# Optimization experiments

Hardware: AMD Instinct MI355X
Metric: run time of the kernel (lower is better)

## Reference

```python
import jax, jax.numpy as jnp
import numpy as np

N = 20000   # nodes
E = 160000  # edges
IN = 16     # in_channels
H = 32      # hidden_channels
MID = 32    # edge-MLP hidden width


def setup_inputs() -> dict:
    key = jax.random.key(0)
    ks = jax.random.split(key, 18)
    s = 0.1  # param scale
    return {
        "x": jax.random.normal(ks[0], (N, IN), jnp.float32),
        "edge_index": jax.random.randint(ks[1], (2, E), 0, N, dtype=jnp.int64),
        "edge_weight": jax.random.uniform(ks[2], (E,), jnp.float32),
        # edge_net1: Linear(1,32) -> SiLU -> Linear(32, IN*H)
        "en1_w1": jax.random.normal(ks[3], (1, MID), jnp.float32) * s,
        "en1_b1": jax.random.normal(ks[4], (MID,), jnp.float32) * s,
        "en1_w2": jax.random.normal(ks[5], (MID, IN * H), jnp.float32) * s,
        "en1_b2": jax.random.normal(ks[6], (IN * H,), jnp.float32) * s,
        "root1": jax.random.normal(ks[7], (IN, H), jnp.float32) * s,
        "bias1": jax.random.normal(ks[8], (H,), jnp.float32) * s,
        # edge_net2: Linear(1,32) -> SiLU -> Linear(32, H*H)
        "en2_w1": jax.random.normal(ks[9], (1, MID), jnp.float32) * s,
        "en2_b1": jax.random.normal(ks[10], (MID,), jnp.float32) * s,
        "en2_w2": jax.random.normal(ks[11], (MID, H * H), jnp.float32) * s,
        "en2_b2": jax.random.normal(ks[12], (H * H,), jnp.float32) * s,
        "root2": jax.random.normal(ks[13], (H, H), jnp.float32) * s,
        "bias2": jax.random.normal(ks[14], (H,), jnp.float32) * s,
        "dec_w": jax.random.normal(ks[15], (H, 1), jnp.float32) * s,
        "dec_b": jax.random.normal(ks[16], (1,), jnp.float32) * s,
    }


def _nnconv(x, src, dst, inv_cnt, e, w1, b1, w2, b2, root, bias, cin, cout):
    # edge MLP -> per-edge [cin, cout] weight matrix
    h = jax.nn.silu(e @ w1 + b1)            # [E, MID]
    w = (h @ w2 + b2).reshape(-1, cin, cout)  # [E, cin, cout]
    msg = jnp.einsum('ei,eio->eo', x[src], w)  # per-edge matmul [E, cout]
    agg = jax.ops.segment_sum(msg, dst, num_segments=N) * inv_cnt  # scatter-mean
    return agg + x @ root + bias


def reference(x, edge_index, edge_weight,
              en1_w1, en1_b1, en1_w2, en1_b2, root1, bias1,
              en2_w1, en2_b1, en2_w2, en2_b2, root2, bias2,
              dec_w, dec_b):
    src, dst = edge_index[0], edge_index[1]
    e = edge_weight[:, None]  # [E, 1]
    cnt = jax.ops.segment_sum(jnp.ones((E,), x.dtype), dst, num_segments=N)
    inv_cnt = (1.0 / jnp.maximum(cnt, 1.0))[:, None]  # [N, 1]
    h = _nnconv(x, src, dst, inv_cnt, e, en1_w1, en1_b1, en1_w2, en1_b2, root1, bias1, IN, H)
    h = jax.nn.silu(h)
    h = _nnconv(h, src, dst, inv_cnt, e, en2_w1, en2_b1, en2_w2, en2_b2, root2, bias2, H, H)
    h = jax.nn.silu(h)
    out = h @ dec_w + dec_b  # [N, 1]
    return out[:, 0]
```

## Files before the change

kernel.cpp:

```cpp
#include <hip/hip_runtime.h>
#include <hip/hip_bf16.h>

#define NN 20000
#define EE 160000
#define HH 32
#define MIDD 32

typedef _Float16 f16x4 __attribute__((ext_vector_type(4)));
typedef _Float16 f16x8 __attribute__((ext_vector_type(8)));
typedef float f32x4 __attribute__((ext_vector_type(4)));

__device__ __forceinline__ float silu_f(float v) {
    return __fdividef(v, 1.0f + __expf(-v));
}

__device__ __forceinline__ void gload_lds_b32(const void* gsrc, void* ldst) {
    __builtin_amdgcn_global_load_lds(
        (const __attribute__((address_space(1))) void*)gsrc,
        (__attribute__((address_space(3))) void*)ldst, 4, 0, 0);
}


__global__ void count_kernel(const int* __restrict__ ei, int* __restrict__ cnt) {
    int e = blockIdx.x * 256 + threadIdx.x;
    if (e < EE) atomicAdd(&cnt[ei[EE + e]], 1);
}

__global__ __launch_bounds__(1024) void scan_kernel(
    const int* __restrict__ cnt, int* __restrict__ off,
    int* __restrict__ cur, float* __restrict__ invc) {
    const int t = threadIdx.x;
    const int base = t * 20;
    __shared__ int wtot[16];

    int c[20];
    if (base + 20 <= NN) {
        const int4* p = (const int4*)(cnt + base);
        #pragma unroll
        for (int q = 0; q < 5; ++q) *(int4*)&c[4 * q] = p[q];
    } else {
        #pragma unroll
        for (int r = 0; r < 20; ++r) {
            int idx = base + r;
            c[r] = (idx < NN) ? cnt[idx] : 0;
        }
    }

    int loc[20];
    int s = 0;
    #pragma unroll
    for (int r = 0; r < 20; ++r) { loc[r] = s; s += c[r]; }

    const int lane = t & 63, wv = t >> 6;
    int incl = s;
    #pragma unroll
    for (int d2 = 1; d2 < 64; d2 <<= 1) {
        int u = __shfl_up(incl, d2);
        if (lane >= d2) incl += u;
    }
    if (lane == 63) wtot[wv] = incl;
    __syncthreads();
    int wbase = 0;
    for (int p2 = 0; p2 < wv; ++p2) wbase += wtot[p2];

    const int excl = wbase + incl - s;

    int o[20];
    #pragma unroll
    for (int r = 0; r < 20; ++r) o[r] = excl + loc[r];
    float iv[20];
    #pragma unroll
    for (int r = 0; r < 20; ++r) iv[r] = 1.0f / fmaxf((float)c[r], 1.0f);

    if (base + 20 <= NN) {
        #pragma unroll
        for (int q = 0; q < 5; ++q) {
            ((int4*)(off + base))[q]    = *(const int4*)&o[4 * q];
            ((int4*)(cur + base))[q]    = *(const int4*)&o[4 * q];
            ((float4*)(invc + base))[q] = *(const float4*)&iv[4 * q];
        }
    } else {
        #pragma unroll
        for (int r = 0; r < 20; ++r) {
            int idx = base + r;
            if (idx < NN) { off[idx] = o[r]; cur[idx] = o[r]; invc[idx] = iv[r]; }
        }
    }
    if (t == 0) off[NN] = EE;
}

__global__ void scatter_kernel(const int* __restrict__ ei, const float* __restrict__ ewt,
                               int* __restrict__ cur,
                               int* __restrict__ ssrc, float* __restrict__ sew) {
    int e = blockIdx.x * 256 + threadIdx.x;
    if (e < EE) {
        int d = ei[EE + e];
        int pos = atomicAdd(&cur[d], 1);
        ssrc[pos] = ei[e];
        sew[pos] = ewt[e];
    }
}

__global__ void build_wt(const float* __restrict__ w2a, const float* __restrict__ b2a,
                         const float* __restrict__ ra,
                         const float* __restrict__ w2b, const float* __restrict__ b2b,
                         const float* __restrict__ rb,
                         _Float16* __restrict__ Wt1, _Float16* __restrict__ Wt2) {
    int idx = blockIdx.x * 256 + threadIdx.x;
    if (idx < 17408) {
        int o = idx / 544, k = idx % 544;
        float v;
        if (k < 512) {
            int m = k & 31, i = k >> 5;
            v = w2a[m * 512 + i * 32 + o];
        } else if (k < 528) {
            v = b2a[(k - 512) * 32 + o];
        } else {
            v = ra[(k - 528) * 32 + o];
        }
        Wt1[o * 544 + k] = (_Float16)v;
    } else if (idx < 52224) {
        int j = idx - 17408;
        int o = j / 1088, k = j % 1088;
        float v;
        if (k < 1024) {
            int m = k & 31, i = k >> 5;
            v = w2b[m * 1024 + i * 32 + o];
        } else if (k < 1056) {
            v = b2b[(k - 1024) * 32 + o];
        } else {
            v = rb[(k - 1056) * 32 + o];
        }
        Wt2[o * 1088 + k] = (_Float16)v;
    }
}


template <int CIN, bool DECODE>
__global__ __launch_bounds__(512, 4) void fused_layer(
    const float* __restrict__ xin, const int* __restrict__ ssrc,
    const float* __restrict__ sew, const int* __restrict__ off,
    const float* __restrict__ invc, const float* __restrict__ w1,
    const float* __restrict__ b1, const _Float16* __restrict__ Wt,
    const float* __restrict__ bias, float* __restrict__ outp,
    const float* __restrict__ dw, const float* __restrict__ db) {
    constexpr int K = 34 * CIN;
    constexpr int LDK = K + 4;
    constexpr int JS = (32 * CIN) / 64;
    constexpr int NQ = JS / 4;
    constexpr int steps = K / 32;
    constexpr int CAP = 256;
    constexpr int RPG = 64 / CIN;

    extern __shared__ char smem[];
    _Float16* Fl = (_Float16*)smem;
    float* pool = (float*)(smem + (size_t)16 * LDK * 2);
    int*   Is = (int*)pool;
    float* Es = pool + CAP;
    float* Xs = pool + 2 * CAP;
    float* red = pool;

    const int t = threadIdx.x;
    const int n0 = blockIdx.x * 16;
    const int lane = t & 63, w = t >> 6;

    const int E0 = off[n0];
    const int E1 = off[n0 + 16];
    const int L = E1 - E0;
    const int Lc = (L < CAP) ? L : CAP;

    if (w == 0) {
        for (int c = 0; c < Lc; c += 64) {
            int idx = c + lane; idx = (idx < L - 1) ? idx : (L - 1);
            gload_lds_b32(ssrc + E0 + idx, Is + c);
        }
    } else if (w == 1) {
        for (int c = 0; c < Lc; c += 64) {
            int idx = c + lane; idx = (idx < L - 1) ? idx : (L - 1);
            gload_lds_b32(sew + E0 + idx, Es + c);
        }
    }
    __syncthreads();

    {
        const int G = (Lc + RPG - 1) / RPG;
        const int er = lane / CIN;
        const int ec = lane & (CIN - 1);
        for (int p = w; p < G; p += 8) {
            int el = p * RPG + er; el = (el < Lc - 1) ? el : (Lc - 1);
            int sn = Is[el];
            gload_lds_b32(xin + (size_t)sn * CIN + ec,
                          Xs + (size_t)p * RPG * CIN);
        }
    }
    __syncthreads();

    {
        const int m = lane & 31;
        const int ihalf = (lane >> 5) * JS;
        const int i0 = lane & (CIN - 1);
        const float w1v = w1[m];
        const float b1v = b1[m];

        for (int c = 0; c < 2; ++c) {
            const int nsub = w * 2 + c;
            const int d = n0 + nsub;
            float Sacc[JS];
            #pragma unroll
            for (int j = 0; j < JS; ++j) Sacc[j] = 0.f;
            float S0 = 0.f;

            const int e0l = off[d] - E0, e1l = off[d + 1] - E0;
            const int eL = (e1l < Lc) ? e1l : Lc;
            const float iv = invc[d];

            #pragma unroll 2
            for (int el = e0l; el < eL; ++el) {
                const float ew = Es[el];
                const float hv = silu_f(fmaf(ew, w1v, b1v));
                const int rb = el * CIN;
                float4 xv[NQ];
                #pragma unroll
                for (int q = 0; q < NQ; ++q)
                    xv[q] = *(const float4*)&Xs[rb + ihalf + 4 * q];
                #pragma unroll
                for (int q = 0; q < NQ; ++q) {
                    Sacc[4 * q + 0] = fmaf(hv, xv[q].x, Sacc[4 * q + 0]);
                    Sacc[4 * q + 1] = fmaf(hv, xv[q].y, Sacc[4 * q + 1]);
                    Sacc[4 * q + 2] = fmaf(hv, xv[q].z, Sacc[4 * q + 2]);
                    Sacc[4 * q + 3] = fmaf(hv, xv[q].w, Sacc[4 * q + 3]);
                }
                S0 += Xs[rb + i0];
            }
            for (int el = eL; el < e1l; ++el) {
                const int sn2 = ssrc[E0 + el];
                const float ew2 = sew[E0 + el];
                const float hv2 = silu_f(fmaf(ew2, w1v, b1v));
                const float* xrow = xin + (size_t)sn2 * CIN;
                #pragma unroll
                for (int q = 0; q < NQ; ++q) {
                    float4 xq = *(const float4*)(xrow + ihalf + 4 * q);
                    Sacc[4 * q + 0] = fmaf(hv2, xq.x, Sacc[4 * q + 0]);
                    Sacc[4 * q + 1] = fmaf(hv2, xq.y, Sacc[4 * q + 1]);
                    Sacc[4 * q + 2] = fmaf(hv2, xq.z, Sacc[4 * q + 2]);
                    Sacc[4 * q + 3] = fmaf(hv2, xq.w, Sacc[4 * q + 3]);
                }
                S0 += xrow[i0];
            }

            _Float16* Fr = Fl + (size_t)nsub * LDK;
            #pragma unroll
            for (int j = 0; j < JS; ++j)
                Fr[(ihalf + j) * 32 + m] = (_Float16)(Sacc[j] * iv);
            if (lane < CIN)
                Fr[32 * CIN + lane] = (_Float16)(S0 * iv);
            else if (lane < 2 * CIN)
                Fr[32 * CIN + lane] = (_Float16)xin[(size_t)d * CIN + (lane - CIN)];
        }
    }
    __syncthreads();

    const int o16 = lane & 15, g = lane >> 4;

    const _Float16* Arow = Fl + (size_t)o16 * LDK + g * 4;
    const _Float16* B0 = Wt + (size_t)o16 * K + g * 4;
    const _Float16* B1 = Wt + (size_t)(o16 + 16) * K + g * 4;

    f32x4 acc0 = {0.f, 0.f, 0.f, 0.f};
    f32x4 acc1 = {0.f, 0.f, 0.f, 0.f};

    const int sb = (steps * w) >> 3;
    const int se = (steps * (w + 1)) >> 3;
    #pragma unroll 2
    for (int s = sb; s < se; ++s) {
        const int k0 = s * 32;
        f16x4 alo = *(const f16x4*)(Arow + k0);
        f16x4 ahi = *(const f16x4*)(Arow + k0 + 16);
        f16x4 b0l = *(const f16x4*)(B0 + k0);
        f16x4 b0h = *(const f16x4*)(B0 + k0 + 16);
        f16x4 b1l = *(const f16x4*)(B1 + k0);
        f16x4 b1h = *(const f16x4*)(B1 + k0 + 16);
        f16x8 a, bb0, bb1;
        #pragma unroll
        for (int j = 0; j < 4; ++j) {
            a[j] = alo[j];  a[j + 4] = ahi[j];
            bb0[j] = b0l[j]; bb0[j + 4] = b0h[j];
            bb1[j] = b1l[j]; bb1[j + 4] = b1h[j];
        }
        acc0 = __builtin_amdgcn_mfma_f32_16x16x32_f16(a, bb0, acc0, 0, 0, 0);
        acc1 = __builtin_amdgcn_mfma_f32_16x16x32_f16(a, bb1, acc1, 0, 0, 0);
    }

    if (w > 0) {
        float* rw = red + (w - 1) * 512;
        #pragma unroll
        for (int r = 0; r < 4; ++r) {
            rw[(g * 4 + r) * 32 + o16]      = acc0[r];
            rw[(g * 4 + r) * 32 + 16 + o16] = acc1[r];
        }
    }
    __syncthreads();
    if (w == 0) {
        #pragma unroll
        for (int r = 0; r < 4; ++r) {
            const int ro = (g * 4 + r) * 32 + o16;
            #pragma unroll
            for (int p = 0; p < 7; ++p) {
                acc0[r] += red[p * 512 + ro];
                acc1[r] += red[p * 512 + ro + 16];
            }
        }
        const float bb0 = bias[o16], bb1 = bias[o16 + 16];
        const int nrow = n0 + g * 4;
        if (!DECODE) {
            #pragma unroll
            for (int r = 0; r < 4; ++r) {
                outp[(size_t)(nrow + r) * 32 + o16]      = silu_f(acc0[r] + bb0);
                outp[(size_t)(nrow + r) * 32 + 16 + o16] = silu_f(acc1[r] + bb1);
            }
        } else {
            const float w0 = dw[o16], w1v = dw[o16 + 16];
            const float dbv = db[0];
            #pragma unroll
            for (int r = 0; r < 4; ++r) {
                float p = silu_f(acc0[r] + bb0) * w0 + silu_f(acc1[r] + bb1) * w1v;
                p += __shfl_xor(p, 1);
                p += __shfl_xor(p, 2);
                p += __shfl_xor(p, 4);
                p += __shfl_xor(p, 8);
                if (o16 == 0) outp[nrow + r] = p + dbv;
            }
        }
    }
}


extern "C" void kernel_launch(void* const* d_in, const int* in_sizes, int n_in,
                              void* d_out, int out_size, void* d_ws, size_t ws_size,
                              hipStream_t stream) {
    const float* x      = (const float*)d_in[0];
    const int*   ei     = (const int*)d_in[1];
    const float* ew     = (const float*)d_in[2];
    const float* en1_w1 = (const float*)d_in[3];
    const float* en1_b1 = (const float*)d_in[4];
    const float* en1_w2 = (const float*)d_in[5];
    const float* en1_b2 = (const float*)d_in[6];
    const float* root1  = (const float*)d_in[7];
    const float* bias1  = (const float*)d_in[8];
    const float* en2_w1 = (const float*)d_in[9];
    const float* en2_b1 = (const float*)d_in[10];
    const float* en2_w2 = (const float*)d_in[11];
    const float* en2_b2 = (const float*)d_in[12];
    const float* root2  = (const float*)d_in[13];
    const float* bias2  = (const float*)d_in[14];
    const float* dec_w  = (const float*)d_in[15];
    const float* dec_b  = (const float*)d_in[16];
    float* out = (float*)d_out;
    (void)in_sizes; (void)n_in; (void)out_size; (void)ws_size;

    char* wp = (char*)d_ws;
    auto alloc = [&](size_t bytes) {
        char* p = wp;
        wp += (bytes + 255) & ~(size_t)255;
        return p;
    };
    int*      cnt  = (int*)alloc((size_t)NN * 4);
    int*      off  = (int*)alloc((size_t)(NN + 1) * 4);
    int*      cur  = (int*)alloc((size_t)NN * 4);
    float*    invc = (float*)alloc((size_t)NN * 4);
    int*      ssrc = (int*)alloc((size_t)EE * 4);
    float*    sew  = (float*)alloc((size_t)EE * 4);
    float*    h1   = (float*)alloc((size_t)NN * 32 * 4);
    _Float16* Wt1  = (_Float16*)alloc((size_t)17408 * 2);
    _Float16* Wt2  = (_Float16*)alloc((size_t)34816 * 2);

    hipMemsetAsync(cnt, 0, (size_t)NN * 4, stream);

    count_kernel<<<(EE + 255) / 256, 256, 0, stream>>>(ei, cnt);
    scan_kernel<<<1, 1024, 0, stream>>>(cnt, off, cur, invc);
    scatter_kernel<<<(EE + 255) / 256, 256, 0, stream>>>(ei, ew, cur, ssrc, sew);
    build_wt<<<(52224 + 255) / 256, 256, 0, stream>>>(en1_w2, en1_b2, root1,
                                                      en2_w2, en2_b2, root2, Wt1, Wt2);

    auto f1 = fused_layer<16, false>;
    auto f2 = fused_layer<32, true>;
    (void)hipFuncSetAttribute((const void*)f1,
                              hipFuncAttributeMaxDynamicSharedMemorySize, 163840);
    (void)hipFuncSetAttribute((const void*)f2,
                              hipFuncAttributeMaxDynamicSharedMemorySize, 163840);

    const size_t lds1 = (size_t)16 * (34 * 16 + 4) * 2 + (size_t)256 * 18 * 4;
    const size_t lds2 = (size_t)16 * (34 * 32 + 4) * 2 + (size_t)256 * 34 * 4;

    fused_layer<16, false><<<NN / 16, 512, lds1, stream>>>(
        x, ssrc, sew, off, invc, en1_w1, en1_b1, Wt1, bias1, h1, nullptr, nullptr);
    fused_layer<32, true><<<NN / 16, 512, lds2, stream>>>(
        h1, ssrc, sew, off, invc, en2_w1, en2_b1, Wt2, bias2, out, dec_w, dec_b);
}
```

Before: 102.0 us.

## Store node features in fp16 to halve gather traffic and LDS footprint

Converts the input features to fp16 in the weight-prep kernel and has layer 1 write its hidden output in fp16. Both fused layers then gather fp16 rows into LDS and accumulate in fp32, which halves gather bytes and staging memory. The edge cap drops from 256 to 192 and the occupancy hint rises from 4 to 6 blocks. The cost is reduced feature precision and more edges going through the slower uncached global fallback path.

```diff
diff --git a/kernel.cpp b/kernel.cpp
--- a/kernel.cpp
+++ b/kernel.cpp
@@ -105,7 +105,9 @@
                          const float* __restrict__ ra,
                          const float* __restrict__ w2b, const float* __restrict__ b2b,
                          const float* __restrict__ rb,
-                         _Float16* __restrict__ Wt1, _Float16* __restrict__ Wt2) {
+                         const float* __restrict__ x,
+                         _Float16* __restrict__ Wt1, _Float16* __restrict__ Wt2,
+                         _Float16* __restrict__ x16) {
     int idx = blockIdx.x * 256 + threadIdx.x;
     if (idx < 17408) {
         int o = idx / 544, k = idx % 544;
@@ -132,32 +134,36 @@
             v = rb[(k - 1056) * 32 + o];
         }
         Wt2[o * 1088 + k] = (_Float16)v;
+    } else if (idx < 52224 + NN * 16) {
+        int j = idx - 52224;
+        x16[j] = (_Float16)x[j];
     }
 }
 
 
 template <int CIN, bool DECODE>
-__global__ __launch_bounds__(512, 4) void fused_layer(
-    const float* __restrict__ xin, const int* __restrict__ ssrc,
+__global__ __launch_bounds__(512, 6) void fused_layer(
+    const _Float16* __restrict__ xin16, const int* __restrict__ ssrc,
     const float* __restrict__ sew, const int* __restrict__ off,
     const float* __restrict__ invc, const float* __restrict__ w1,
     const float* __restrict__ b1, const _Float16* __restrict__ Wt,
-    const float* __restrict__ bias, float* __restrict__ outp,
+    const float* __restrict__ bias, void* __restrict__ outp,
     const float* __restrict__ dw, const float* __restrict__ db) {
     constexpr int K = 34 * CIN;
     constexpr int LDK = K + 4;
     constexpr int JS = (32 * CIN) / 64;
-    constexpr int NQ = JS / 4;
+    constexpr int NH = JS / 8;
     constexpr int steps = K / 32;
-    constexpr int CAP = 256;
-    constexpr int RPG = 64 / CIN;
+    constexpr int CAP = 192;
+    constexpr int RPG = 128 / CIN;
+    constexpr int LPR = CIN / 2;
 
     extern __shared__ char smem[];
     _Float16* Fl = (_Float16*)smem;
     float* pool = (float*)(smem + (size_t)16 * LDK * 2);
     int*   Is = (int*)pool;
     float* Es = pool + CAP;
-    float* Xs = pool + 2 * CAP;
+    _Float16* Xs = (_Float16*)(pool + 2 * CAP);
     float* red = pool;
 
     const int t = threadIdx.x;
@@ -184,12 +190,12 @@
 
     {
         const int G = (Lc + RPG - 1) / RPG;
-        const int er = lane / CIN;
-        const int ec = lane & (CIN - 1);
+        const int er = lane / LPR;
+        const int ecp = lane % LPR;
         for (int p = w; p < G; p += 8) {
             int el = p * RPG + er; el = (el < Lc - 1) ? el : (Lc - 1);
             int sn = Is[el];
-            gload_lds_b32(xin + (size_t)sn * CIN + ec,
+            gload_lds_b32(xin16 + (size_t)sn * CIN + 2 * ecp,
                           Xs + (size_t)p * RPG * CIN);
         }
     }
@@ -219,33 +225,30 @@
                 const float ew = Es[el];
                 const float hv = silu_f(fmaf(ew, w1v, b1v));
                 const int rb = el * CIN;
-                float4 xv[NQ];
+                f16x8 xh[NH];
                 #pragma unroll
-                for (int q = 0; q < NQ; ++q)
-                    xv[q] = *(const float4*)&Xs[rb + ihalf + 4 * q];
+                for (int q = 0; q < NH; ++q)
+                    xh[q] = *(const f16x8*)&Xs[rb + ihalf + 8 * q];
                 #pragma unroll
-                for (int q = 0; q < NQ; ++q) {
-                    Sacc[4 * q + 0] = fmaf(hv, xv[q].x, Sacc[4 * q + 0]);
-                    Sacc[4 * q + 1] = fmaf(hv, xv[q].y, Sacc[4 * q + 1]);
-                    Sacc[4 * q + 2] = fmaf(hv, xv[q].z, Sacc[4 * q + 2]);
-                    Sacc[4 * q + 3] = fmaf(hv, xv[q].w, Sacc[4 * q + 3]);
-                }
-                S0 += Xs[rb + i0];
+                for (int q = 0; q < NH; ++q)
+                    #pragma unroll
+                    for (int j = 0; j < 8; ++j)
+                        Sacc[8 * q + j] = fmaf((float)xh[q][j], hv, Sacc[8 * q + j]);
+                S0 += (float)Xs[rb + i0];
             }
             for (int el = eL; el < e1l; ++el) {
                 const int sn2 = ssrc[E0 + el];
                 const float ew2 = sew[E0 + el];
                 const float hv2 = silu_f(fmaf(ew2, w1v, b1v));
-                const float* xrow = xin + (size_t)sn2 * CIN;
+                const _Float16* xrow = xin16 + (size_t)sn2 * CIN;
                 #pragma unroll
-                for (int q = 0; q < NQ; ++q) {
-                    float4 xq = *(const float4*)(xrow + ihalf + 4 * q);
-                    Sacc[4 * q + 0] = fmaf(hv2, xq.x, Sacc[4 * q + 0]);
-                    Sacc[4 * q + 1] = fmaf(hv2, xq.y, Sacc[4 * q + 1]);
-                    Sacc[4 * q + 2] = fmaf(hv2, xq.z, Sacc[4 * q + 2]);
-                    Sacc[4 * q + 3] = fmaf(hv2, xq.w, Sacc[4 * q + 3]);
+                for (int q = 0; q < NH; ++q) {
+                    f16x8 xq = *(const f16x8*)(xrow + ihalf + 8 * q);
+                    #pragma unroll
+                    for (int j = 0; j < 8; ++j)
+                        Sacc[8 * q + j] = fmaf((float)xq[j], hv2, Sacc[8 * q + j]);
                 }
-                S0 += xrow[i0];
+                S0 += (float)xrow[i0];
             }
 
             _Float16* Fr = Fl + (size_t)nsub * LDK;
@@ -255,7 +258,7 @@
             if (lane < CIN)
                 Fr[32 * CIN + lane] = (_Float16)(S0 * iv);
             else if (lane < 2 * CIN)
-                Fr[32 * CIN + lane] = (_Float16)xin[(size_t)d * CIN + (lane - CIN)];
+                Fr[32 * CIN + lane] = xin16[(size_t)d * CIN + (lane - CIN)];
         }
     }
     __syncthreads();
@@ -313,12 +316,14 @@
         const float bb0 = bias[o16], bb1 = bias[o16 + 16];
         const int nrow = n0 + g * 4;
         if (!DECODE) {
+            _Float16* op = (_Float16*)outp;
             #pragma unroll
             for (int r = 0; r < 4; ++r) {
-                outp[(size_t)(nrow + r) * 32 + o16]      = silu_f(acc0[r] + bb0);
-                outp[(size_t)(nrow + r) * 32 + 16 + o16] = silu_f(acc1[r] + bb1);
+                op[(size_t)(nrow + r) * 32 + o16]      = (_Float16)silu_f(acc0[r] + bb0);
+                op[(size_t)(nrow + r) * 32 + 16 + o16] = (_Float16)silu_f(acc1[r] + bb1);
             }
         } else {
+            float* op = (float*)outp;
             const float w0 = dw[o16], w1v = dw[o16 + 16];
             const float dbv = db[0];
             #pragma unroll
@@ -328,7 +333,7 @@
                 p += __shfl_xor(p, 2);
                 p += __shfl_xor(p, 4);
                 p += __shfl_xor(p, 8);
-                if (o16 == 0) outp[nrow + r] = p + dbv;
+                if (o16 == 0) op[nrow + r] = p + dbv;
             }
         }
     }
@@ -370,7 +375,8 @@
     float*    invc = (float*)alloc((size_t)NN * 4);
     int*      ssrc = (int*)alloc((size_t)EE * 4);
     float*    sew  = (float*)alloc((size_t)EE * 4);
-    float*    h1   = (float*)alloc((size_t)NN * 32 * 4);
+    _Float16* h1h  = (_Float16*)alloc((size_t)NN * 32 * 2);
+    _Float16* x16  = (_Float16*)alloc((size_t)NN * 16 * 2);
     _Float16* Wt1  = (_Float16*)alloc((size_t)17408 * 2);
     _Float16* Wt2  = (_Float16*)alloc((size_t)34816 * 2);
 
@@ -379,8 +385,8 @@
     count_kernel<<<(EE + 255) / 256, 256, 0, stream>>>(ei, cnt);
     scan_kernel<<<1, 1024, 0, stream>>>(cnt, off, cur, invc);
     scatter_kernel<<<(EE + 255) / 256, 256, 0, stream>>>(ei, ew, cur, ssrc, sew);
-    build_wt<<<(52224 + 255) / 256, 256, 0, stream>>>(en1_w2, en1_b2, root1,
-                                                      en2_w2, en2_b2, root2, Wt1, Wt2);
+    build_wt<<<(52224 + NN * 16 + 255) / 256, 256, 0, stream>>>(
+        en1_w2, en1_b2, root1, en2_w2, en2_b2, root2, x, Wt1, Wt2, x16);
 
     auto f1 = fused_layer<16, false>;
     auto f2 = fused_layer<32, true>;
@@ -389,11 +395,11 @@
     (void)hipFuncSetAttribute((const void*)f2,
                               hipFuncAttributeMaxDynamicSharedMemorySize, 163840);
 
-    const size_t lds1 = (size_t)16 * (34 * 16 + 4) * 2 + (size_t)256 * 18 * 4;
-    const size_t lds2 = (size_t)16 * (34 * 32 + 4) * 2 + (size_t)256 * 34 * 4;
+    const size_t lds1 = (size_t)16 * (34 * 16 + 4) * 2 + 14336;
+    const size_t lds2 = (size_t)16 * (34 * 32 + 4) * 2 + 14336;
 
     fused_layer<16, false><<<NN / 16, 512, lds1, stream>>>(
-        x, ssrc, sew, off, invc, en1_w1, en1_b1, Wt1, bias1, h1, nullptr, nullptr);
+        x16, ssrc, sew, off, invc, en1_w1, en1_b1, Wt1, bias1, h1h, nullptr, nullptr);
     fused_layer<32, true><<<NN / 16, 512, lds2, stream>>>(
-        h1, ssrc, sew, off, invc, en2_w1, en2_b1, Wt2, bias2, out, dec_w, dec_b);
-}
+        h1h, ssrc, sew, off, invc, en2_w1, en2_b1, Wt2, bias2, out, dec_w, dec_b);
+}
```

New measurement: 103.3 us. About the same (+1.3%).
